# Performance work log

Hardware: AMD Instinct MI355X
Metric: run time of the kernel (lower is better)

## Reference

```python
import jax, jax.numpy as jnp
import numpy as np

D_MODEL = 256
D_FF = 1024
N_HEADS = 4
D_K = D_MODEL // N_HEADS
RMS_EPS = 1e-5
B, T = 4, 2048


def setup_inputs() -> dict:
    key = jax.random.key(0)
    ks = jax.random.split(key, 12)
    s = 0.02
    inp = {
        "x": jax.random.normal(ks[0], (B, T, D_MODEL), dtype=jnp.float32),
        # causal lower-triangular mask (True = attend)
        "causal_mask": jnp.tril(jnp.ones((1, 1, T, T), dtype=bool)),
        "rms_attn_w": jnp.ones((D_MODEL,), jnp.float32),
        "wq": jax.random.normal(ks[1], (D_MODEL, D_MODEL), jnp.float32) * s,
        "wk": jax.random.normal(ks[2], (D_MODEL, D_MODEL), jnp.float32) * s,
        "wv": jax.random.normal(ks[3], (D_MODEL, D_MODEL), jnp.float32) * s,
        "wo": jax.random.normal(ks[4], (D_MODEL, D_MODEL), jnp.float32) * s,
        "rms_ffn_w": jnp.ones((D_MODEL,), jnp.float32),
        "w_gate": jax.random.normal(ks[5], (D_FF, D_MODEL), jnp.float32) * s,
        "w_up": jax.random.normal(ks[6], (D_FF, D_MODEL), jnp.float32) * s,
        "w_down": jax.random.normal(ks[7], (D_MODEL, D_FF), jnp.float32) * s,
    }
    return inp


def _rmsnorm(x, w):
    rms = jnp.sqrt(jnp.mean(x * x, axis=-1, keepdims=True) + RMS_EPS)
    return x / rms * w


def reference(x, causal_mask, rms_attn_w, wq, wk, wv, wo, rms_ffn_w, w_gate, w_up, w_down):
    b, t, c = x.shape
    h = _rmsnorm(x, rms_attn_w)
    # torch Linear: y = x @ W.T, W is [out, in]
    q = (h @ wq.T).reshape(b, t, N_HEADS, D_K).transpose(0, 2, 1, 3)  # [B,H,T,Dk]
    k = (h @ wk.T).reshape(b, t, N_HEADS, D_K).transpose(0, 2, 1, 3)
    v = (h @ wv.T).reshape(b, t, N_HEADS, D_K).transpose(0, 2, 1, 3)
    scores = jnp.einsum("bhqd,bhkd->bhqk", q, k) / jnp.sqrt(jnp.float32(D_K))
    scores = jnp.where(causal_mask[:, :, :t, :t], scores, jnp.float32(-jnp.inf))
    attn = jax.nn.softmax(scores, axis=-1)
    out = jnp.einsum("bhqk,bhkd->bhqd", attn, v).transpose(0, 2, 1, 3).reshape(b, t, c)
    x = x + out @ wo.T
    hf = _rmsnorm(x, rms_ffn_w)
    ffn = (jax.nn.silu(hf @ w_gate.T) * (hf @ w_up.T)) @ w_down.T
    return x + ffn
```

## Files before the change

### kernel.cpp

```cpp
#include <hip/hip_runtime.h>
#include <hip/hip_bf16.h>
#include <math.h>

#define TT 2048
typedef __bf16 bf16x8 __attribute__((ext_vector_type(8)));
typedef float f32x4 __attribute__((ext_vector_type(4)));
typedef __hip_bfloat16 bf16;

static __device__ __forceinline__ f32x4 mfma16(bf16x8 a, bf16x8 b, f32x4 c) {
  return __builtin_amdgcn_mfma_f32_16x16x32_bf16(a, b, c, 0, 0, 0);
}
static __device__ __forceinline__ bf16x8 ldb8(const bf16* p) {
  return *(const bf16x8*)p;
}
static __device__ __forceinline__ void gll16(const bf16* g, bf16* l) {
  __builtin_amdgcn_global_load_lds(
      (const __attribute__((address_space(1))) unsigned int*)g,
      (__attribute__((address_space(3))) unsigned int*)l, 16, 0, 0);
}

__global__ void __launch_bounds__(256) prep_kernel(
    const float* __restrict__ wq, const float* __restrict__ wk,
    const float* __restrict__ wv, const float* __restrict__ wo,
    const float* __restrict__ wg, const float* __restrict__ wu,
    const float* __restrict__ wd,
    bf16* __restrict__ Wqkv, bf16* __restrict__ Wo,
    bf16* __restrict__ Wgu, bf16* __restrict__ Wd,
    const float* __restrict__ x, const float* __restrict__ rmsw,
    bf16* __restrict__ hb) {
  if (blockIdx.x < 4096) {
    int idx = blockIdx.x * 256 + threadIdx.x;
    if (idx < 196608) {
      int row = idx >> 8, col = idx & 255;
      const float* src = row < 256 ? wq : (row < 512 ? wk : wv);
      Wqkv[idx] = __float2bfloat16(src[(row & 255) * 256 + col]);
    } else if (idx < 262144) {
      int i = idx - 196608;
      Wo[i] = __float2bfloat16(wo[i]);
    } else if (idx < 786432) {
      int i = idx - 262144;
      int row = i >> 8, col = i & 255;
      int t = row >> 4, r = row & 15;
      int f = (t >> 1) * 16 + r;
      const float* src = (t & 1) ? wu : wg;
      Wgu[i] = __float2bfloat16(src[f * 256 + col]);
    } else {
      int i = idx - 786432;
      Wd[i] = __float2bfloat16(wd[i]);
    }
  } else {
    const int wv_ = threadIdx.x >> 6, lane = threadIdx.x & 63;
    const int token = (blockIdx.x - 4096) * 4 + wv_;
    const float4 xv = ((const float4*)x)[token * 64 + lane];
    float ss = xv.x * xv.x + xv.y * xv.y + xv.z * xv.z + xv.w * xv.w;
#pragma unroll
    for (int off = 1; off < 64; off <<= 1) ss += __shfl_xor(ss, off, 64);
    const float inv = rsqrtf(ss * (1.0f / 256.0f) + 1e-5f);
    const float4 w4 = ((const float4*)rmsw)[lane];
    union { unsigned short u[4]; uint2 v2; } pk;
    bf16 b0 = __float2bfloat16(xv.x * inv * w4.x);
    bf16 b1 = __float2bfloat16(xv.y * inv * w4.y);
    bf16 b2 = __float2bfloat16(xv.z * inv * w4.z);
    bf16 b3 = __float2bfloat16(xv.w * inv * w4.w);
    pk.u[0] = *(unsigned short*)&b0; pk.u[1] = *(unsigned short*)&b1;
    pk.u[2] = *(unsigned short*)&b2; pk.u[3] = *(unsigned short*)&b3;
    ((uint2*)hb)[token * 64 + lane] = pk.v2;
  }
}

__global__ void __launch_bounds__(256) rmsnorm_kernel(
    const float* __restrict__ x, const float* __restrict__ w, bf16* __restrict__ out) {
  const int wv = threadIdx.x >> 6, lane = threadIdx.x & 63;
  const int token = blockIdx.x * 4 + wv;
  const float4 xv = ((const float4*)x)[token * 64 + lane];
  float ss = xv.x * xv.x + xv.y * xv.y + xv.z * xv.z + xv.w * xv.w;
#pragma unroll
  for (int off = 1; off < 64; off <<= 1) ss += __shfl_xor(ss, off, 64);
  const float inv = rsqrtf(ss * (1.0f / 256.0f) + 1e-5f);
  const float4 w4 = ((const float4*)w)[lane];
  union { unsigned short u[4]; uint2 v2; } pk;
  bf16 b0 = __float2bfloat16(xv.x * inv * w4.x);
  bf16 b1 = __float2bfloat16(xv.y * inv * w4.y);
  bf16 b2 = __float2bfloat16(xv.z * inv * w4.z);
  bf16 b3 = __float2bfloat16(xv.w * inv * w4.w);
  pk.u[0] = *(unsigned short*)&b0; pk.u[1] = *(unsigned short*)&b1;
  pk.u[2] = *(unsigned short*)&b2; pk.u[3] = *(unsigned short*)&b3;
  ((uint2*)out)[token * 64 + lane] = pk.v2;
}

template <int BM, int BN>
static __device__ __forceinline__ void gemm_lds_loop(
    const bf16* __restrict__ Ag, const bf16* __restrict__ Bg,
    int lda, int ldb, int ktot,
    bf16* ldsA, bf16* ldsB, int wave, int lane,
    f32x4 (&acc)[BM / 32][BN / 32]) {
  const int lo = lane & 15, hi = lane >> 4;
  const int wm = (wave >> 1) * (BM / 2), wn = (wave & 1) * (BN / 2);
  const int lrow = lane >> 2, lcol = (lane & 3) * 8;
  for (int k0 = 0; k0 < ktot; k0 += 32) {
    __syncthreads();
    for (int is = wave; is < BM / 16; is += 4)
      gll16(Ag + (size_t)(is * 16 + lrow) * lda + k0 + lcol, ldsA + is * 512);
    for (int is = wave; is < BN / 16; is += 4)
      gll16(Bg + (size_t)(is * 16 + lrow) * ldb + k0 + lcol, ldsB + is * 512);
    __syncthreads();
    bf16x8 af[BM / 32], bfr[BN / 32];
#pragma unroll
    for (int i = 0; i < BM / 32; i++)
      af[i] = ldb8(ldsA + (wm + i * 16 + lo) * 32 + hi * 8);
#pragma unroll
    for (int j = 0; j < BN / 32; j++)
      bfr[j] = ldb8(ldsB + (wn + j * 16 + lo) * 32 + hi * 8);
#pragma unroll
    for (int i = 0; i < BM / 32; i++)
#pragma unroll
      for (int j = 0; j < BN / 32; j++)
        acc[i][j] = mfma16(af[i], bfr[j], acc[i][j]);
  }
}

__global__ void __launch_bounds__(256) qkv_gemm(
    const bf16* __restrict__ A, const bf16* __restrict__ W,
    bf16* __restrict__ qb, bf16* __restrict__ kb, bf16* __restrict__ vtb) {
  __shared__ __align__(16) bf16 ldsA[64 * 32], ldsB[128 * 32];
  const int wave = threadIdx.x >> 6, lane = threadIdx.x & 63;
  const int lo = lane & 15, hi = lane >> 4;
  const int wm = (wave >> 1) * 32, wn = (wave & 1) * 64;
  f32x4 acc[2][4];
#pragma unroll
  for (int i = 0; i < 2; i++)
#pragma unroll
    for (int j = 0; j < 4; j++) acc[i][j] = (f32x4){0.f, 0.f, 0.f, 0.f};
  gemm_lds_loop<64, 128>(A + (size_t)blockIdx.x * 64 * 256, W + (size_t)blockIdx.y * 128 * 256,
                         256, 256, 256, ldsA, ldsB, wave, lane, acc);
#pragma unroll
  for (int i = 0; i < 2; i++)
#pragma unroll
    for (int j = 0; j < 4; j++) {
      const int o = blockIdx.y * 128 + wn + j * 16 + lo;
      const int sel = o >> 8, hd = (o >> 6) & 3, d = o & 63;
#pragma unroll
      for (int r = 0; r < 4; r++) {
        const int m = blockIdx.x * 64 + wm + i * 16 + hi * 4 + r;
        const int b = m >> 11, t = m & (TT - 1);
        const int bh = b * 4 + hd;
        const float v = acc[i][j][r];
        if (sel == 0)      qb[((size_t)bh * TT + t) * 64 + d] = __float2bfloat16(v * 0.125f);
        else if (sel == 1) kb[((size_t)bh * TT + t) * 64 + d] = __float2bfloat16(v);
        else               vtb[((size_t)bh * 64 + d) * TT + t] = __float2bfloat16(v);
      }
    }
}

__global__ void __launch_bounds__(256) attn_kernel(
    const bf16* __restrict__ qbp, const bf16* __restrict__ kbp,
    const bf16* __restrict__ vtp, bf16* __restrict__ aout) {
  const int wave = threadIdx.x >> 6, lane = threadIdx.x & 63;
  const int lo = lane & 15, hi = lane >> 4;
  const int bh = blockIdx.y;
  __shared__ __align__(16) unsigned short ldsP[4][2][16][40];
  __shared__ __align__(16) unsigned short ldsO[4][32][88];
  __shared__ float ldsL[4][2][16];
  const bf16* Q  = qbp + (size_t)bh * (TT * 64);
  const bf16* Kp = kbp + (size_t)bh * (TT * 64);
  const bf16* Vt = vtp + (size_t)bh * (64 * TT);
  const int b = bh >> 2, hd = bh & 3;

  for (int half = 0; half < 2; half++) {
    const int qt = half == 0 ? (int)blockIdx.x : 63 - (int)blockIdx.x;
    const int q0 = qt * 32;
    const int ns = qt + 1;
    bf16x8 aq[2][2];
#pragma unroll
    for (int mf = 0; mf < 2; mf++)
#pragma unroll
      for (int h = 0; h < 2; h++)
        aq[mf][h] = ldb8(Q + (q0 + mf * 16 + lo) * 64 + h * 32 + hi * 8);
    f32x4 acc[2][4];
#pragma unroll
    for (int mf = 0; mf < 2; mf++)
#pragma unroll
      for (int dt = 0; dt < 4; dt++) acc[mf][dt] = (f32x4){0.f, 0.f, 0.f, 0.f};
    float lsum[2] = {0.f, 0.f};

    int i = wave;
    bf16x8 kf[2][2];
    if (i < ns) {
#pragma unroll
      for (int ct = 0; ct < 2; ct++) {
        const bf16* kr = Kp + (i * 32 + ct * 16 + lo) * 64 + hi * 8;
        kf[ct][0] = ldb8(kr);
        kf[ct][1] = ldb8(kr + 32);
      }
    }
    for (; i < ns; i += 4) {
      const int kt0 = i * 32;
      f32x4 s[2][2];
#pragma unroll
      for (int mf = 0; mf < 2; mf++)
#pragma unroll
        for (int ct = 0; ct < 2; ct++) {
          f32x4 sc = (f32x4){0.f, 0.f, 0.f, 0.f};
          sc = mfma16(kf[ct][0], aq[mf][0], sc);
          sc = mfma16(kf[ct][1], aq[mf][1], sc);
          s[mf][ct] = sc;
        }
      const int ktn = (i + 4 < ns ? i + 4 : i) * 32;
      bf16x8 kn[2][2];
#pragma unroll
      for (int ct = 0; ct < 2; ct++) {
        const bf16* kr = Kp + (ktn + ct * 16 + lo) * 64 + hi * 8;
        kn[ct][0] = ldb8(kr);
        kn[ct][1] = ldb8(kr + 32);
      }
      bf16x8 vb[4];
#pragma unroll
      for (int dt = 0; dt < 4; dt++)
        vb[dt] = ldb8(Vt + (dt * 16 + lo) * TT + kt0 + hi * 8);
      if (i == ns - 1) {
#pragma unroll
        for (int mf = 0; mf < 2; mf++)
#pragma unroll
          for (int ct = 0; ct < 2; ct++)
#pragma unroll
            for (int r = 0; r < 4; r++)
              if (kt0 + ct * 16 + hi * 4 + r > q0 + mf * 16 + lo) s[mf][ct][r] = -INFINITY;
      }
#pragma unroll
      for (int mf = 0; mf < 2; mf++)
#pragma unroll
        for (int ct = 0; ct < 2; ct++) {
          union { unsigned short u[4]; uint2 v2; } pk;
#pragma unroll
          for (int r = 0; r < 4; r++) {
            const float p = __expf(s[mf][ct][r]);
            lsum[mf] += p;
            bf16 pb = __float2bfloat16(p);
            pk.u[r] = *(unsigned short*)&pb;
          }
          *(uint2*)&ldsP[wave][mf][lo][ct * 16 + hi * 4] = pk.v2;
        }
      asm volatile("s_waitcnt lgkmcnt(0)" ::: "memory");
      bf16x8 pa[2];
#pragma unroll
      for (int mf = 0; mf < 2; mf++)
        pa[mf] = *(const bf16x8*)&ldsP[wave][mf][lo][hi * 8];
#pragma unroll
      for (int mf = 0; mf < 2; mf++)
#pragma unroll
        for (int dt = 0; dt < 4; dt++)
          acc[mf][dt] = mfma16(vb[dt], pa[mf], acc[mf][dt]);
#pragma unroll
      for (int ct = 0; ct < 2; ct++) {
        kf[ct][0] = kn[ct][0];
        kf[ct][1] = kn[ct][1];
      }
    }

#pragma unroll
    for (int mf = 0; mf < 2; mf++) {
      lsum[mf] += __shfl_xor(lsum[mf], 16, 64);
      lsum[mf] += __shfl_xor(lsum[mf], 32, 64);
    }
    if (hi == 0) {
      ldsL[wave][0][lo] = lsum[0];
      ldsL[wave][1][lo] = lsum[1];
    }
#pragma unroll
    for (int mf = 0; mf < 2; mf++)
#pragma unroll
      for (int dt = 0; dt < 4; dt++) {
        union { unsigned short u[4]; uint2 v2; } pk;
#pragma unroll
        for (int r = 0; r < 4; r++) {
          bf16 ob = __float2bfloat16(acc[mf][dt][r]);
          pk.u[r] = *(unsigned short*)&ob;
        }
        *(uint2*)&ldsO[wave][mf * 16 + lo][dt * 16 + hi * 4] = pk.v2;
      }
    __syncthreads();

    const int q = threadIdx.x >> 3;
    const int d0 = (threadIdx.x & 7) * 8;
    const float L = ldsL[0][q >> 4][q & 15] + ldsL[1][q >> 4][q & 15] +
                    ldsL[2][q >> 4][q & 15] + ldsL[3][q >> 4][q & 15];
    float o[8] = {0.f, 0.f, 0.f, 0.f, 0.f, 0.f, 0.f, 0.f};
#pragma unroll
    for (int w = 0; w < 4; w++) {
      const bf16x8 v = *(const bf16x8*)&ldsO[w][q][d0];
#pragma unroll
      for (int j = 0; j < 8; j++) o[j] += (float)v[j];
    }
    const float invL = 1.0f / L;
    bf16* dst = aout + ((size_t)(b * TT + q0 + q)) * 256 + hd * 64 + d0;
    union { unsigned short u[8]; uint4 v4; } pk;
#pragma unroll
    for (int j = 0; j < 8; j++) {
      bf16 ob = __float2bfloat16(o[j] * invL);
      pk.u[j] = *(unsigned short*)&ob;
    }
    *(uint4*)dst = pk.v4;
    __syncthreads();
  }
}

__global__ void __launch_bounds__(256) wo_gemm(
    const bf16* __restrict__ A, const bf16* __restrict__ W,
    const float* __restrict__ x, float* __restrict__ x2) {
  __shared__ __align__(16) bf16 ldsA[64 * 32], ldsB[64 * 32];
  const int wave = threadIdx.x >> 6, lane = threadIdx.x & 63;
  const int lo = lane & 15, hi = lane >> 4;
  const int wm = (wave >> 1) * 32, wn = (wave & 1) * 32;
  f32x4 acc[2][2];
#pragma unroll
  for (int i = 0; i < 2; i++)
#pragma unroll
    for (int j = 0; j < 2; j++) acc[i][j] = (f32x4){0.f, 0.f, 0.f, 0.f};
  gemm_lds_loop<64, 64>(A + (size_t)blockIdx.x * 64 * 256, W + (size_t)blockIdx.y * 64 * 256,
                        256, 256, 256, ldsA, ldsB, wave, lane, acc);
#pragma unroll
  for (int i = 0; i < 2; i++)
#pragma unroll
    for (int j = 0; j < 2; j++) {
      const int col = blockIdx.y * 64 + wn + j * 16 + lo;
#pragma unroll
      for (int r = 0; r < 4; r++) {
        const size_t idx = (size_t)(blockIdx.x * 64 + wm + i * 16 + hi * 4 + r) * 256 + col;
        x2[idx] = x[idx] + acc[i][j][r];
      }
    }
}

__global__ void __launch_bounds__(256) gu_gemm(
    const bf16* __restrict__ A, const bf16* __restrict__ W, bf16* __restrict__ mid) {
  __shared__ __align__(16) bf16 ldsA[128 * 32], ldsB[128 * 32];
  const int wave = threadIdx.x >> 6, lane = threadIdx.x & 63;
  const int lo = lane & 15, hi = lane >> 4;
  const int wm = (wave >> 1) * 64, wn = (wave & 1) * 64;
  f32x4 acc[4][4];
#pragma unroll
  for (int i = 0; i < 4; i++)
#pragma unroll
    for (int j = 0; j < 4; j++) acc[i][j] = (f32x4){0.f, 0.f, 0.f, 0.f};
  gemm_lds_loop<128, 128>(A + (size_t)blockIdx.x * 128 * 256, W + (size_t)blockIdx.y * 128 * 256,
                          256, 256, 256, ldsA, ldsB, wave, lane, acc);
#pragma unroll
  for (int i = 0; i < 4; i++)
#pragma unroll
    for (int jp = 0; jp < 2; jp++) {
      const int f = (blockIdx.y * 4 + (wn >> 5) + jp) * 16 + lo;
#pragma unroll
      for (int r = 0; r < 4; r++) {
        const int m = blockIdx.x * 128 + wm + i * 16 + hi * 4 + r;
        const float g = acc[i][2 * jp][r];
        const float u = acc[i][2 * jp + 1][r];
        const float sv = g / (1.f + __expf(-g)) * u;
        mid[(size_t)m * 1024 + f] = __float2bfloat16(sv);
      }
    }
}

__global__ void __launch_bounds__(256) down_gemm(
    const bf16* __restrict__ A, const bf16* __restrict__ W,
    const float* __restrict__ x2, float* __restrict__ out) {
  __shared__ __align__(16) bf16 ldsA[64 * 32], ldsB[64 * 32];
  const int wave = threadIdx.x >> 6, lane = threadIdx.x & 63;
  const int lo = lane & 15, hi = lane >> 4;
  const int wm = (wave >> 1) * 32, wn = (wave & 1) * 32;
  f32x4 acc[2][2];
#pragma unroll
  for (int i = 0; i < 2; i++)
#pragma unroll
    for (int j = 0; j < 2; j++) acc[i][j] = (f32x4){0.f, 0.f, 0.f, 0.f};
  gemm_lds_loop<64, 64>(A + (size_t)blockIdx.x * 64 * 1024, W + (size_t)blockIdx.y * 64 * 1024,
                        1024, 1024, 1024, ldsA, ldsB, wave, lane, acc);
#pragma unroll
  for (int i = 0; i < 2; i++)
#pragma unroll
    for (int j = 0; j < 2; j++) {
      const int col = blockIdx.y * 64 + wn + j * 16 + lo;
#pragma unroll
      for (int r = 0; r < 4; r++) {
        const size_t idx = (size_t)(blockIdx.x * 64 + wm + i * 16 + hi * 4 + r) * 256 + col;
        out[idx] = x2[idx] + acc[i][j][r];
      }
    }
}

extern "C" void kernel_launch(void* const* d_in, const int* in_sizes, int n_in,
                              void* d_out, int out_size, void* d_ws, size_t ws_size,
                              hipStream_t stream) {
  const float* x          = (const float*)d_in[0];
  const float* rms_attn_w = (const float*)d_in[2];
  const float* wq         = (const float*)d_in[3];
  const float* wk         = (const float*)d_in[4];
  const float* wv         = (const float*)d_in[5];
  const float* wo         = (const float*)d_in[6];
  const float* rms_ffn_w  = (const float*)d_in[7];
  const float* wg         = (const float*)d_in[8];
  const float* wu         = (const float*)d_in[9];
  const float* wd         = (const float*)d_in[10];
  float* out = (float*)d_out;
  char* ws = (char*)d_ws;

  bf16* Wqkv  = (bf16*)(ws + 0);
  bf16* Wo    = (bf16*)(ws + 393216);
  bf16* Wgu   = (bf16*)(ws + 524288);
  bf16* Wd    = (bf16*)(ws + 1572864);
  bf16* hb    = (bf16*)(ws + 2097152);
  bf16* qb    = (bf16*)(ws + 6291456);
  bf16* kb    = (bf16*)(ws + 10485760);
  bf16* vtb   = (bf16*)(ws + 14680064);
  bf16* attnb = (bf16*)(ws + 18874368);
  float* x2   = (float*)(ws + 23068672);
  bf16* h2b   = (bf16*)(ws + 31457280);
  bf16* midb  = (bf16*)(ws + 35651584);

  hipLaunchKernelGGL(prep_kernel, dim3(6144), dim3(256), 0, stream,
                     wq, wk, wv, wo, wg, wu, wd, Wqkv, Wo, Wgu, Wd,
                     x, rms_attn_w, hb);
  hipLaunchKernelGGL(qkv_gemm, dim3(128, 6), dim3(256), 0, stream, hb, Wqkv, qb, kb, vtb);
  hipLaunchKernelGGL(attn_kernel, dim3(32, 16), dim3(256), 0, stream, qb, kb, vtb, attnb);
  hipLaunchKernelGGL(wo_gemm, dim3(128, 4), dim3(256), 0, stream, attnb, Wo, x, x2);
  hipLaunchKernelGGL(rmsnorm_kernel, dim3(2048), dim3(256), 0, stream, x2, rms_ffn_w, h2b);
  hipLaunchKernelGGL(gu_gemm, dim3(64, 16), dim3(256), 0, stream, h2b, Wgu, midb);
  hipLaunchKernelGGL(down_gemm, dim3(128, 4), dim3(256), 0, stream, midb, Wd, x2, out);
}
```

Measured before the change: 182.5 us.

## Load multiple K-chunks per barrier in GEMMs and retile QKV projection

The shared GEMM loop now stages several 32-wide K slices (128 or 256) into LDS between each pair of barriers instead of one slice per iteration. This cuts the number of __syncthreads and exposed load latencies per K sweep. The QKV GEMM is also retiled from 64x128 to 128x64 blocks with a matching grid change. The trade-off is much larger LDS footprints per block (up to 64 KB), which can lower occupancy.

```diff
diff --git a/kernel.cpp b/kernel.cpp
--- a/kernel.cpp
+++ b/kernel.cpp
@@ -88,8 +88,8 @@
   ((uint2*)out)[token * 64 + lane] = pk.v2;
 }
 
-template <int BM, int BN>
-static __device__ __forceinline__ void gemm_lds_loop(
+template <int BM, int BN, int KC>
+static __device__ __forceinline__ void gemm_chunks(
     const bf16* __restrict__ Ag, const bf16* __restrict__ Bg,
     int lda, int ldb, int ktot,
     bf16* ldsA, bf16* ldsB, int wave, int lane,
@@ -97,51 +97,60 @@
   const int lo = lane & 15, hi = lane >> 4;
   const int wm = (wave >> 1) * (BM / 2), wn = (wave & 1) * (BN / 2);
   const int lrow = lane >> 2, lcol = (lane & 3) * 8;
-  for (int k0 = 0; k0 < ktot; k0 += 32) {
+  for (int kc = 0; kc < ktot; kc += KC) {
     __syncthreads();
-    for (int is = wave; is < BM / 16; is += 4)
-      gll16(Ag + (size_t)(is * 16 + lrow) * lda + k0 + lcol, ldsA + is * 512);
-    for (int is = wave; is < BN / 16; is += 4)
-      gll16(Bg + (size_t)(is * 16 + lrow) * ldb + k0 + lcol, ldsB + is * 512);
+#pragma unroll
+    for (int c = 0; c < KC / 32; c++) {
+      for (int is = wave; is < BM / 16; is += 4)
+        gll16(Ag + (size_t)(is * 16 + lrow) * lda + kc + c * 32 + lcol,
+              ldsA + c * (BM * 32) + is * 512);
+      for (int is = wave; is < BN / 16; is += 4)
+        gll16(Bg + (size_t)(is * 16 + lrow) * ldb + kc + c * 32 + lcol,
+              ldsB + c * (BN * 32) + is * 512);
+    }
     __syncthreads();
-    bf16x8 af[BM / 32], bfr[BN / 32];
-#pragma unroll
-    for (int i = 0; i < BM / 32; i++)
-      af[i] = ldb8(ldsA + (wm + i * 16 + lo) * 32 + hi * 8);
-#pragma unroll
-    for (int j = 0; j < BN / 32; j++)
-      bfr[j] = ldb8(ldsB + (wn + j * 16 + lo) * 32 + hi * 8);
-#pragma unroll
-    for (int i = 0; i < BM / 32; i++)
+#pragma unroll
+    for (int c = 0; c < KC / 32; c++) {
+      bf16x8 af[BM / 32], bfr[BN / 32];
+#pragma unroll
+      for (int i = 0; i < BM / 32; i++)
+        af[i] = ldb8(ldsA + c * (BM * 32) + (wm + i * 16 + lo) * 32 + hi * 8);
 #pragma unroll
       for (int j = 0; j < BN / 32; j++)
-        acc[i][j] = mfma16(af[i], bfr[j], acc[i][j]);
+        bfr[j] = ldb8(ldsB + c * (BN * 32) + (wn + j * 16 + lo) * 32 + hi * 8);
+#pragma unroll
+      for (int i = 0; i < BM / 32; i++)
+#pragma unroll
+        for (int j = 0; j < BN / 32; j++)
+          acc[i][j] = mfma16(af[i], bfr[j], acc[i][j]);
+    }
   }
 }
 
 __global__ void __launch_bounds__(256) qkv_gemm(
     const bf16* __restrict__ A, const bf16* __restrict__ W,
     bf16* __restrict__ qb, bf16* __restrict__ kb, bf16* __restrict__ vtb) {
-  __shared__ __align__(16) bf16 ldsA[64 * 32], ldsB[128 * 32];
+  __shared__ __align__(16) bf16 ldsA[128 * 128], ldsB[64 * 128];
   const int wave = threadIdx.x >> 6, lane = threadIdx.x & 63;
   const int lo = lane & 15, hi = lane >> 4;
-  const int wm = (wave >> 1) * 32, wn = (wave & 1) * 64;
-  f32x4 acc[2][4];
-#pragma unroll
-  for (int i = 0; i < 2; i++)
-#pragma unroll
-    for (int j = 0; j < 4; j++) acc[i][j] = (f32x4){0.f, 0.f, 0.f, 0.f};
-  gemm_lds_loop<64, 128>(A + (size_t)blockIdx.x * 64 * 256, W + (size_t)blockIdx.y * 128 * 256,
-                         256, 256, 256, ldsA, ldsB, wave, lane, acc);
-#pragma unroll
-  for (int i = 0; i < 2; i++)
-#pragma unroll
-    for (int j = 0; j < 4; j++) {
-      const int o = blockIdx.y * 128 + wn + j * 16 + lo;
+  const int wm = (wave >> 1) * 64, wn = (wave & 1) * 32;
+  f32x4 acc[4][2];
+#pragma unroll
+  for (int i = 0; i < 4; i++)
+#pragma unroll
+    for (int j = 0; j < 2; j++) acc[i][j] = (f32x4){0.f, 0.f, 0.f, 0.f};
+  gemm_chunks<128, 64, 128>(A + (size_t)blockIdx.x * 128 * 256,
+                            W + (size_t)blockIdx.y * 64 * 256,
+                            256, 256, 256, ldsA, ldsB, wave, lane, acc);
+#pragma unroll
+  for (int i = 0; i < 4; i++)
+#pragma unroll
+    for (int j = 0; j < 2; j++) {
+      const int o = blockIdx.y * 64 + wn + j * 16 + lo;
       const int sel = o >> 8, hd = (o >> 6) & 3, d = o & 63;
 #pragma unroll
       for (int r = 0; r < 4; r++) {
-        const int m = blockIdx.x * 64 + wm + i * 16 + hi * 4 + r;
+        const int m = blockIdx.x * 128 + wm + i * 16 + hi * 4 + r;
         const int b = m >> 11, t = m & (TT - 1);
         const int bh = b * 4 + hd;
         const float v = acc[i][j][r];
@@ -307,7 +316,7 @@
 __global__ void __launch_bounds__(256) wo_gemm(
     const bf16* __restrict__ A, const bf16* __restrict__ W,
     const float* __restrict__ x, float* __restrict__ x2) {
-  __shared__ __align__(16) bf16 ldsA[64 * 32], ldsB[64 * 32];
+  __shared__ __align__(16) bf16 ldsA[64 * 256], ldsB[64 * 256];
   const int wave = threadIdx.x >> 6, lane = threadIdx.x & 63;
   const int lo = lane & 15, hi = lane >> 4;
   const int wm = (wave >> 1) * 32, wn = (wave & 1) * 32;
@@ -316,8 +325,9 @@
   for (int i = 0; i < 2; i++)
 #pragma unroll
     for (int j = 0; j < 2; j++) acc[i][j] = (f32x4){0.f, 0.f, 0.f, 0.f};
-  gemm_lds_loop<64, 64>(A + (size_t)blockIdx.x * 64 * 256, W + (size_t)blockIdx.y * 64 * 256,
-                        256, 256, 256, ldsA, ldsB, wave, lane, acc);
+  gemm_chunks<64, 64, 256>(A + (size_t)blockIdx.x * 64 * 256,
+                           W + (size_t)blockIdx.y * 64 * 256,
+                           256, 256, 256, ldsA, ldsB, wave, lane, acc);
 #pragma unroll
   for (int i = 0; i < 2; i++)
 #pragma unroll
@@ -333,7 +343,7 @@
 
 __global__ void __launch_bounds__(256) gu_gemm(
     const bf16* __restrict__ A, const bf16* __restrict__ W, bf16* __restrict__ mid) {
-  __shared__ __align__(16) bf16 ldsA[128 * 32], ldsB[128 * 32];
+  __shared__ __align__(16) bf16 ldsA[128 * 128], ldsB[128 * 128];
   const int wave = threadIdx.x >> 6, lane = threadIdx.x & 63;
   const int lo = lane & 15, hi = lane >> 4;
   const int wm = (wave >> 1) * 64, wn = (wave & 1) * 64;
@@ -342,8 +352,9 @@
   for (int i = 0; i < 4; i++)
 #pragma unroll
     for (int j = 0; j < 4; j++) acc[i][j] = (f32x4){0.f, 0.f, 0.f, 0.f};
-  gemm_lds_loop<128, 128>(A + (size_t)blockIdx.x * 128 * 256, W + (size_t)blockIdx.y * 128 * 256,
-                          256, 256, 256, ldsA, ldsB, wave, lane, acc);
+  gemm_chunks<128, 128, 128>(A + (size_t)blockIdx.x * 128 * 256,
+                             W + (size_t)blockIdx.y * 128 * 256,
+                             256, 256, 256, ldsA, ldsB, wave, lane, acc);
 #pragma unroll
   for (int i = 0; i < 4; i++)
 #pragma unroll
@@ -363,7 +374,7 @@
 __global__ void __launch_bounds__(256) down_gemm(
     const bf16* __restrict__ A, const bf16* __restrict__ W,
     const float* __restrict__ x2, float* __restrict__ out) {
-  __shared__ __align__(16) bf16 ldsA[64 * 32], ldsB[64 * 32];
+  __shared__ __align__(16) bf16 ldsA[64 * 256], ldsB[64 * 256];
   const int wave = threadIdx.x >> 6, lane = threadIdx.x & 63;
   const int lo = lane & 15, hi = lane >> 4;
   const int wm = (wave >> 1) * 32, wn = (wave & 1) * 32;
@@ -372,8 +383,9 @@
   for (int i = 0; i < 2; i++)
 #pragma unroll
     for (int j = 0; j < 2; j++) acc[i][j] = (f32x4){0.f, 0.f, 0.f, 0.f};
-  gemm_lds_loop<64, 64>(A + (size_t)blockIdx.x * 64 * 1024, W + (size_t)blockIdx.y * 64 * 1024,
-                        1024, 1024, 1024, ldsA, ldsB, wave, lane, acc);
+  gemm_chunks<64, 64, 256>(A + (size_t)blockIdx.x * 64 * 1024,
+                           W + (size_t)blockIdx.y * 64 * 1024,
+                           1024, 1024, 1024, ldsA, ldsB, wave, lane, acc);
 #pragma unroll
   for (int i = 0; i < 2; i++)
 #pragma unroll
@@ -419,7 +431,7 @@
   hipLaunchKernelGGL(prep_kernel, dim3(6144), dim3(256), 0, stream,
                      wq, wk, wv, wo, wg, wu, wd, Wqkv, Wo, Wgu, Wd,
                      x, rms_attn_w, hb);
-  hipLaunchKernelGGL(qkv_gemm, dim3(128, 6), dim3(256), 0, stream, hb, Wqkv, qb, kb, vtb);
+  hipLaunchKernelGGL(qkv_gemm, dim3(64, 12), dim3(256), 0, stream, hb, Wqkv, qb, kb, vtb);
   hipLaunchKernelGGL(attn_kernel, dim3(32, 16), dim3(256), 0, stream, qb, kb, vtb, attnb);
   hipLaunchKernelGGL(wo_gemm, dim3(128, 4), dim3(256), 0, stream, attnb, Wo, x, x2);
   hipLaunchKernelGGL(rmsnorm_kernel, dim3(2048), dim3(256), 0, stream, x2, rms_ffn_w, h2b);
```

New measurement: 172.1 us. 1.06x faster.
